# Optimization experiments

Hardware: AMD Instinct MI355X
Metric: run time of the kernel (lower is better)

Reference implementation:

```python
import jax, jax.numpy as jnp
import numpy as np

B, T, I, H, O = 128, 512, 512, 2048, 512  # batch, seq_length, input, hidden, output


def setup_inputs() -> dict:
    key = jax.random.key(0)
    ks = jax.random.split(key, 8)
    s_ih = 1.0 / np.sqrt(H)  # torch RNNCell/Linear default init scale 1/sqrt(hidden)
    body = jax.random.normal(ks[0], (B, T - 1, I), dtype=jnp.float32)
    # last timestep row stores the integer pad index (as float), per the module's protocol
    pad = jax.random.randint(ks[1], (B,), 0, T - 2)
    last = jnp.broadcast_to(pad[:, None, None].astype(jnp.float32), (B, 1, I))
    x = jnp.concatenate([body, last], axis=1)  # [B, T, I]
    W_ih = jax.random.uniform(ks[2], (H, I), jnp.float32, -s_ih, s_ih)
    W_hh = jax.random.uniform(ks[3], (H, H), jnp.float32, -s_ih, s_ih)
    b_ih = jax.random.uniform(ks[4], (H,), jnp.float32, -s_ih, s_ih)
    b_hh = jax.random.uniform(ks[5], (H,), jnp.float32, -s_ih, s_ih)
    W_fc = jax.random.uniform(ks[6], (O, H), jnp.float32, -s_ih, s_ih)
    b_fc = jax.random.uniform(ks[7], (O,), jnp.float32, -s_ih, s_ih)
    h0 = jnp.ones((H,), jnp.float32)  # self.h parameter, ones-initialized
    return {"x": x, "h0": h0, "W_ih": W_ih, "b_ih": b_ih, "W_hh": W_hh,
            "b_hh": b_hh, "W_fc": W_fc, "b_fc": b_fc}


def reference(x, h0, W_ih, b_ih, W_hh, b_hh, W_fc, b_fc):
    steps = T - 2  # loop runs over x.shape[2]-1 = (T-1)-1 timesteps
    pad = x[:, -1, 0].astype(jnp.int32)          # [B] pad indices
    xs = jnp.transpose(x[:, :steps, :], (1, 0, 2))  # [steps, B, I]
    h_init = jnp.broadcast_to(h0, (x.shape[0], H))  # self.h * ones([B,1])

    def step(h, xt):
        h = jnp.tanh(xt @ W_ih.T + b_ih + h @ W_hh.T + b_hh)
        return h, h @ W_fc.T + b_fc

    _, outs = jax.lax.scan(step, h_init, xs)     # [steps, B, O]
    # mask selects the single timestep j == pad_len[b]; everything else is zeroed
    mask = (pad[None, :] == jnp.arange(steps)[:, None]).astype(outs.dtype)  # [steps, B]
    return jnp.sum(outs * mask[:, :, None], axis=0)  # [B, O]
```

## Files before the change

kernel.cpp:

```cpp
#include <hip/hip_runtime.h>

#define Bsz 128
#define Tsz 512
#define Isz 512
#define Hsz 2048
#define Osz 512
#define STEPS 510

typedef short short8 __attribute__((ext_vector_type(8)));
typedef float floatx4 __attribute__((ext_vector_type(4)));

__device__ __forceinline__ unsigned short f2bf(float f) {
  unsigned int u = __builtin_bit_cast(unsigned int, f);
  u += 0x7FFFu + ((u >> 16) & 1u);
  return (unsigned short)(u >> 16);
}

__device__ __forceinline__ float tanh_fast(float x) {
  const float e = __expf(2.f * x);
  return 1.f - 2.f * __builtin_amdgcn_rcpf(e + 1.f);
}

template <int AUX>
__device__ __forceinline__ void gload_lds16(const void* g, void* l) {
  __builtin_amdgcn_global_load_lds(
      (const __attribute__((address_space(1))) void*)g,
      (__attribute__((address_space(3))) void*)l, 16, 0, AUX);
}

#define HCHUNK(c, enc)                                                                         \
  {                                                                                            \
    __builtin_amdgcn_s_waitcnt(enc);                                                           \
    const int hb = wvoff + (c) * 1024 + m16 * 64;                                              \
    const short8 a0 = *reinterpret_cast<const short8*>(&h_lds[hb + (quad ^ m7) * 8]);          \
    acc[0] = __builtin_amdgcn_mfma_f32_16x16x32_bf16(a0, wf[(c) * 2][0], acc[0], 0, 0, 0);     \
    acc[1] = __builtin_amdgcn_mfma_f32_16x16x32_bf16(a0, wf[(c) * 2][1], acc[1], 0, 0, 0);     \
    acc[2] = __builtin_amdgcn_mfma_f32_16x16x32_bf16(a0, wf[(c) * 2][2], acc[2], 0, 0, 0);     \
    acc[3] = __builtin_amdgcn_mfma_f32_16x16x32_bf16(a0, wf[(c) * 2][3], acc[3], 0, 0, 0);     \
    const short8 a1 = *reinterpret_cast<const short8*>(&h_lds[hb + ((4 + quad) ^ m7) * 8]);    \
    acc[0] = __builtin_amdgcn_mfma_f32_16x16x32_bf16(a1, wf[(c) * 2 + 1][0], acc[0], 0, 0, 0); \
    acc[1] = __builtin_amdgcn_mfma_f32_16x16x32_bf16(a1, wf[(c) * 2 + 1][1], acc[1], 0, 0, 0); \
    acc[2] = __builtin_amdgcn_mfma_f32_16x16x32_bf16(a1, wf[(c) * 2 + 1][2], acc[2], 0, 0, 0); \
    acc[3] = __builtin_amdgcn_mfma_f32_16x16x32_bf16(a1, wf[(c) * 2 + 1][3], acc[3], 0, 0, 0); \
  }

__global__ __launch_bounds__(256, 1)
void rnn_kernel(const float* __restrict__ x, const float* __restrict__ h0v,
                const float* __restrict__ W_ih, const float* __restrict__ b_ih,
                const float* __restrict__ W_hh, const float* __restrict__ b_hh,
                unsigned short* __restrict__ hbuf,
                float* __restrict__ hfinal,
                unsigned int* __restrict__ flags,
                unsigned int* __restrict__ xcc_arr)
{
  __shared__ short h_lds[4 * 8192];
  __shared__ float red_lds[4 * 1024];
  __shared__ int pad_lds[16];
  __shared__ unsigned int mode_lds;

  const int tid = threadIdx.x;
  const int lane = tid & 63;
  const int wv = tid >> 6;
  const int m16 = lane & 15;
  const int quad = lane >> 4;
  const int m7 = m16 & 7;
  const int rg = blockIdx.x & 7;
  const int cg = blockIdx.x >> 3;
  const int b0 = rg * 16;
  const int c0 = cg * 64;
  const int kq = wv * 512;
  const int kqx = wv * 128;
  const int wvoff = wv * 8192;

  {
    unsigned int xcc;
    asm volatile("s_getreg_b32 %0, hwreg(HW_REG_XCC_ID)" : "=s"(xcc));
    if (tid == 0)
      __hip_atomic_store(&xcc_arr[rg * 32 + cg], xcc + 1u, __ATOMIC_RELAXED,
                         __HIP_MEMORY_SCOPE_AGENT);
    if (wv == 0) {
      const unsigned int* ap = &xcc_arr[rg * 32 + (lane & 31)];
      unsigned int v;
      do {
        v = __hip_atomic_load(ap, __ATOMIC_RELAXED, __HIP_MEMORY_SCOPE_AGENT);
        if (__all((int)(v != 0u))) break;
        __builtin_amdgcn_s_sleep(2);
      } while (true);
      const int same = __all((int)(v == xcc + 1u));
      if (tid == 0) mode_lds = (unsigned int)same;
    }
  }

  short8 wf[16][4];
  short8 wih[4][4];
#pragma unroll
  for (int nt = 0; nt < 4; ++nt) {
    const int wrow = c0 + nt * 16 + m16;
    const float* base = W_hh + (size_t)wrow * Hsz + kq + quad * 8;
#pragma unroll
    for (int kc = 0; kc < 16; ++kc) {
      short8 v;
#pragma unroll
      for (int j = 0; j < 8; ++j) v[j] = (short)f2bf(base[kc * 32 + j]);
      wf[kc][nt] = v;
    }
    const float* basex = W_ih + (size_t)wrow * Isz + kqx + quad * 8;
#pragma unroll
    for (int kc = 0; kc < 4; ++kc) {
      short8 v;
#pragma unroll
      for (int j = 0; j < 8; ++j) v[j] = (short)f2bf(basex[kc * 32 + j]);
      wih[kc][nt] = v;
    }
  }

  const int rrow = tid >> 4;
  const int rcb = (tid & 15) * 4;
  float bias[4];
#pragma unroll
  for (int i = 0; i < 4; ++i) bias[i] = b_ih[c0 + rcb + i] + b_hh[c0 + rcb + i];

  if (tid < 16)
    pad_lds[tid] = (int)x[(size_t)(b0 + tid) * (Tsz * Isz) + (size_t)(Tsz - 1) * Isz];

  for (int i = lane; i < 1024; i += 64) {
    const int c = i >> 7;
    const int r = (i >> 3) & 15;
    const int u = i & 7;
    const int k = kq + c * 64 + u * 8;
    short8 v;
#pragma unroll
    for (int j = 0; j < 8; ++j) v[j] = (short)f2bf(h0v[k + j]);
    *reinterpret_cast<short8*>(&h_lds[wvoff + c * 1024 + r * 64 + (u ^ (r & 7)) * 8]) = v;
  }

  __syncthreads();
  const bool use_l2 = (mode_lds != 0u);

  const unsigned int* fp = flags + (size_t)(wv * 8 + (lane & 7)) * 8 + rg;

  for (int t = 0; t < STEPS; ++t) {
    const bool have_next = (t + 1) < STEPS;

    const float* xp = x + (size_t)(b0 + m16) * (Tsz * Isz) + (size_t)t * Isz + kqx + quad * 8;
    float4 xv[8];
#pragma unroll
    for (int kcc = 0; kcc < 4; ++kcc) {
      xv[2 * kcc] = *reinterpret_cast<const float4*>(xp + kcc * 32);
      xv[2 * kcc + 1] = *reinterpret_cast<const float4*>(xp + kcc * 32 + 4);
    }

    if (t > 0) {
      while (!__all((int)(__hip_atomic_load(fp, __ATOMIC_RELAXED,
                                            __HIP_MEMORY_SCOPE_AGENT) >= (unsigned)t)))
        __builtin_amdgcn_s_sleep(1);
      const unsigned short* hsrcp = hbuf + (size_t)(t & 1) * (Bsz * Hsz);
      if (use_l2) {
#pragma unroll
        for (int c = 0; c < 8; ++c) {
          const unsigned short* src = hsrcp + (size_t)((wv * 8 + c) * 8 + rg) * 1024;
          gload_lds16<0x01>(src + lane * 8, &h_lds[wvoff + c * 1024]);
          gload_lds16<0x01>(src + 512 + lane * 8, &h_lds[wvoff + c * 1024 + 512]);
        }
      } else {
#pragma unroll
        for (int c = 0; c < 8; ++c) {
          const unsigned short* src = hsrcp + (size_t)((wv * 8 + c) * 8 + rg) * 1024;
          gload_lds16<0x11>(src + lane * 8, &h_lds[wvoff + c * 1024]);
          gload_lds16<0x11>(src + 512 + lane * 8, &h_lds[wvoff + c * 1024 + 512]);
        }
      }
    }

    short8 xa[4];
#pragma unroll
    for (int kcc = 0; kcc < 4; ++kcc) {
      short8 a;
      a[0] = (short)f2bf(xv[2 * kcc].x);
      a[1] = (short)f2bf(xv[2 * kcc].y);
      a[2] = (short)f2bf(xv[2 * kcc].z);
      a[3] = (short)f2bf(xv[2 * kcc].w);
      a[4] = (short)f2bf(xv[2 * kcc + 1].x);
      a[5] = (short)f2bf(xv[2 * kcc + 1].y);
      a[6] = (short)f2bf(xv[2 * kcc + 1].z);
      a[7] = (short)f2bf(xv[2 * kcc + 1].w);
      xa[kcc] = a;
    }

    floatx4 acc[4];
#pragma unroll
    for (int nt = 0; nt < 4; ++nt) {
      floatx4 zero = {0.f, 0.f, 0.f, 0.f};
      acc[nt] = zero;
    }
#pragma unroll
    for (int kcc = 0; kcc < 4; ++kcc)
#pragma unroll
      for (int nt = 0; nt < 4; ++nt)
        acc[nt] = __builtin_amdgcn_mfma_f32_16x16x32_bf16(xa[kcc], wih[kcc][nt], acc[nt], 0, 0, 0);

    HCHUNK(0, 0x0F7E)
    HCHUNK(1, 0x0F7C)
    HCHUNK(2, 0x0F7A)
    HCHUNK(3, 0x0F78)
    HCHUNK(4, 0x0F76)
    HCHUNK(5, 0x0F74)
    HCHUNK(6, 0x0F72)
    HCHUNK(7, 0x0F70)

#pragma unroll
    for (int nt = 0; nt < 4; ++nt)
#pragma unroll
      for (int i = 0; i < 4; ++i)
        red_lds[wv * 1024 + (quad * 4 + i) * 64 + nt * 16 + m16] = acc[nt][i];

    __syncthreads();

    {
      float4 z = {0.f, 0.f, 0.f, 0.f};
#pragma unroll
      for (int ww = 0; ww < 4; ++ww) {
        const float4 p =
            *reinterpret_cast<const float4*>(&red_lds[ww * 1024 + rrow * 64 + rcb]);
        z.x += p.x; z.y += p.y; z.z += p.z; z.w += p.w;
      }
      const float t0 = tanh_fast(z.x + bias[0]);
      const float t1 = tanh_fast(z.y + bias[1]);
      const float t2 = tanh_fast(z.z + bias[2]);
      const float t3 = tanh_fast(z.w + bias[3]);
      unsigned long long pk = (unsigned long long)f2bf(t0) |
                              ((unsigned long long)f2bf(t1) << 16) |
                              ((unsigned long long)f2bf(t2) << 32) |
                              ((unsigned long long)f2bf(t3) << 48);
      const int toff = rrow * 64 + ((rcb >> 3) ^ (rrow & 7)) * 8 + ((rcb >> 2) & 1) * 4;
      unsigned short* hd = hbuf + (size_t)((t + 1) & 1) * (Bsz * Hsz) +
                           (size_t)(cg * 8 + rg) * 1024 + toff;
      if (use_l2) {
        *reinterpret_cast<unsigned long long*>(hd) = pk;
      } else {
        __hip_atomic_store(reinterpret_cast<unsigned long long*>(hd), pk,
                           __ATOMIC_RELAXED, __HIP_MEMORY_SCOPE_AGENT);
      }
      if (pad_lds[rrow] == t) {
        float4 o;
        o.x = t0; o.y = t1; o.z = t2; o.w = t3;
        *reinterpret_cast<float4*>(&hfinal[(size_t)(b0 + rrow) * Hsz + c0 + rcb]) = o;
      }
    }

    __syncthreads();

    if (have_next && tid == 0) {
      __hip_atomic_store(flags + cg * 8 + rg, (unsigned)(t + 1),
                         __ATOMIC_RELAXED, __HIP_MEMORY_SCOPE_AGENT);
    }
  }
}

__global__ __launch_bounds__(64)
void fc_kernel(const float* __restrict__ hfinal, const float* __restrict__ W_fc,
               const float* __restrict__ b_fc, float* __restrict__ out) {
  const int lane = threadIdx.x & 63;
  const int m16 = lane & 15;
  const int quad = lane >> 4;
  const int b0 = (blockIdx.x & 7) * 16;
  const int o0 = (blockIdx.x >> 3) * 16;
  floatx4 acc = {0.f, 0.f, 0.f, 0.f};
  const float* ap = hfinal + (size_t)(b0 + m16) * Hsz + quad * 8;
  const float* bp = W_fc + (size_t)(o0 + m16) * Hsz + quad * 8;
#pragma unroll 4
  for (int kc = 0; kc < 64; ++kc) {
    short8 a, b;
#pragma unroll
    for (int j = 0; j < 8; ++j) a[j] = (short)f2bf(ap[kc * 32 + j]);
#pragma unroll
    for (int j = 0; j < 8; ++j) b[j] = (short)f2bf(bp[kc * 32 + j]);
    acc = __builtin_amdgcn_mfma_f32_16x16x32_bf16(a, b, acc, 0, 0, 0);
  }
  const float bias = b_fc[o0 + m16];
#pragma unroll
  for (int i = 0; i < 4; ++i)
    out[(size_t)(b0 + quad * 4 + i) * Osz + o0 + m16] = acc[i] + bias;
}

__global__ void zero_flags(unsigned int* f) { f[blockIdx.x * 256 + threadIdx.x] = 0u; }

extern "C" void kernel_launch(void* const* d_in, const int* in_sizes, int n_in,
                              void* d_out, int out_size, void* d_ws, size_t ws_size,
                              hipStream_t stream) {
  const float* x = (const float*)d_in[0];
  const float* h0 = (const float*)d_in[1];
  const float* W_ih = (const float*)d_in[2];
  const float* b_ih = (const float*)d_in[3];
  const float* W_hh = (const float*)d_in[4];
  const float* b_hh = (const float*)d_in[5];
  const float* W_fc = (const float*)d_in[6];
  const float* b_fc = (const float*)d_in[7];
  float* out = (float*)d_out;

  char* ws = (char*)d_ws;
  unsigned short* hbuf = (unsigned short*)ws;
  float* hfinal = (float*)(ws + (1u << 20));
  unsigned int* flags = (unsigned int*)(ws + (2u << 20));
  unsigned int* xcc_arr = flags + 256;

  zero_flags<<<2, 256, 0, stream>>>(flags);
  rnn_kernel<<<256, 256, 0, stream>>>(x, h0, W_ih, b_ih, W_hh, b_hh, hbuf, hfinal,
                                      flags, xcc_arr);
  fc_kernel<<<256, 64, 0, stream>>>(hfinal, W_fc, b_fc, out);
}
```

Before: 2.069 ms.

## Split RNN block K-reduction across eight waves instead of four

Doubles the threads per block to 512 so each wave handles half the hidden and input reduction slice. Register-resident W_hh/W_ih fragments per wave shrink, and the per-step MFMA chain and h loads per wave halve. The cost is an eight-way LDS cross-wave reduction with narrower float2 epilogue stores, plus more flag polling per wave. Because 512 threads share one CU, the register budget per wave also tightens.

```diff
diff --git a/kernel.cpp b/kernel.cpp
--- a/kernel.cpp
+++ b/kernel.cpp
@@ -44,7 +44,7 @@
     acc[3] = __builtin_amdgcn_mfma_f32_16x16x32_bf16(a1, wf[(c) * 2 + 1][3], acc[3], 0, 0, 0); \
   }
 
-__global__ __launch_bounds__(256, 1)
+__global__ __launch_bounds__(512, 2)
 void rnn_kernel(const float* __restrict__ x, const float* __restrict__ h0v,
                 const float* __restrict__ W_ih, const float* __restrict__ b_ih,
                 const float* __restrict__ W_hh, const float* __restrict__ b_hh,
@@ -53,8 +53,8 @@
                 unsigned int* __restrict__ flags,
                 unsigned int* __restrict__ xcc_arr)
 {
-  __shared__ short h_lds[4 * 8192];
-  __shared__ float red_lds[4 * 1024];
+  __shared__ short h_lds[8 * 4096];
+  __shared__ float red_lds[8 * 1024];
   __shared__ int pad_lds[16];
   __shared__ unsigned int mode_lds;
 
@@ -68,9 +68,9 @@
   const int cg = blockIdx.x >> 3;
   const int b0 = rg * 16;
   const int c0 = cg * 64;
-  const int kq = wv * 512;
-  const int kqx = wv * 128;
-  const int wvoff = wv * 8192;
+  const int kq = wv * 256;
+  const int kqx = wv * 64;
+  const int wvoff = wv * 4096;
 
   {
     unsigned int xcc;
@@ -91,14 +91,14 @@
     }
   }
 
-  short8 wf[16][4];
-  short8 wih[4][4];
+  short8 wf[8][4];
+  short8 wih[2][4];
 #pragma unroll
   for (int nt = 0; nt < 4; ++nt) {
     const int wrow = c0 + nt * 16 + m16;
     const float* base = W_hh + (size_t)wrow * Hsz + kq + quad * 8;
 #pragma unroll
-    for (int kc = 0; kc < 16; ++kc) {
+    for (int kc = 0; kc < 8; ++kc) {
       short8 v;
 #pragma unroll
       for (int j = 0; j < 8; ++j) v[j] = (short)f2bf(base[kc * 32 + j]);
@@ -106,7 +106,7 @@
     }
     const float* basex = W_ih + (size_t)wrow * Isz + kqx + quad * 8;
 #pragma unroll
-    for (int kc = 0; kc < 4; ++kc) {
+    for (int kc = 0; kc < 2; ++kc) {
       short8 v;
 #pragma unroll
       for (int j = 0; j < 8; ++j) v[j] = (short)f2bf(basex[kc * 32 + j]);
@@ -114,16 +114,15 @@
     }
   }
 
-  const int rrow = tid >> 4;
-  const int rcb = (tid & 15) * 4;
-  float bias[4];
-#pragma unroll
-  for (int i = 0; i < 4; ++i) bias[i] = b_ih[c0 + rcb + i] + b_hh[c0 + rcb + i];
+  const int rrow = tid >> 5;
+  const int cb = (tid & 31) * 2;
+  const float bias0 = b_ih[c0 + cb] + b_hh[c0 + cb];
+  const float bias1 = b_ih[c0 + cb + 1] + b_hh[c0 + cb + 1];
 
   if (tid < 16)
     pad_lds[tid] = (int)x[(size_t)(b0 + tid) * (Tsz * Isz) + (size_t)(Tsz - 1) * Isz];
 
-  for (int i = lane; i < 1024; i += 64) {
+  for (int i = lane; i < 512; i += 64) {
     const int c = i >> 7;
     const int r = (i >> 3) & 15;
     const int u = i & 7;
@@ -137,15 +136,15 @@
   __syncthreads();
   const bool use_l2 = (mode_lds != 0u);
 
-  const unsigned int* fp = flags + (size_t)(wv * 8 + (lane & 7)) * 8 + rg;
+  const unsigned int* fp = flags + (size_t)(wv * 4 + (lane & 3)) * 8 + rg;
 
   for (int t = 0; t < STEPS; ++t) {
     const bool have_next = (t + 1) < STEPS;
 
     const float* xp = x + (size_t)(b0 + m16) * (Tsz * Isz) + (size_t)t * Isz + kqx + quad * 8;
-    float4 xv[8];
-#pragma unroll
-    for (int kcc = 0; kcc < 4; ++kcc) {
+    float4 xv[4];
+#pragma unroll
+    for (int kcc = 0; kcc < 2; ++kcc) {
       xv[2 * kcc] = *reinterpret_cast<const float4*>(xp + kcc * 32);
       xv[2 * kcc + 1] = *reinterpret_cast<const float4*>(xp + kcc * 32 + 4);
     }
@@ -157,24 +156,24 @@
       const unsigned short* hsrcp = hbuf + (size_t)(t & 1) * (Bsz * Hsz);
       if (use_l2) {
 #pragma unroll
-        for (int c = 0; c < 8; ++c) {
-          const unsigned short* src = hsrcp + (size_t)((wv * 8 + c) * 8 + rg) * 1024;
+        for (int c = 0; c < 4; ++c) {
+          const unsigned short* src = hsrcp + (size_t)((wv * 4 + c) * 8 + rg) * 1024;
           gload_lds16<0x01>(src + lane * 8, &h_lds[wvoff + c * 1024]);
           gload_lds16<0x01>(src + 512 + lane * 8, &h_lds[wvoff + c * 1024 + 512]);
         }
       } else {
 #pragma unroll
-        for (int c = 0; c < 8; ++c) {
-          const unsigned short* src = hsrcp + (size_t)((wv * 8 + c) * 8 + rg) * 1024;
+        for (int c = 0; c < 4; ++c) {
+          const unsigned short* src = hsrcp + (size_t)((wv * 4 + c) * 8 + rg) * 1024;
           gload_lds16<0x11>(src + lane * 8, &h_lds[wvoff + c * 1024]);
           gload_lds16<0x11>(src + 512 + lane * 8, &h_lds[wvoff + c * 1024 + 512]);
         }
       }
     }
 
-    short8 xa[4];
-#pragma unroll
-    for (int kcc = 0; kcc < 4; ++kcc) {
+    short8 xa[2];
+#pragma unroll
+    for (int kcc = 0; kcc < 2; ++kcc) {
       short8 a;
       a[0] = (short)f2bf(xv[2 * kcc].x);
       a[1] = (short)f2bf(xv[2 * kcc].y);
@@ -194,19 +193,15 @@
       acc[nt] = zero;
     }
 #pragma unroll
-    for (int kcc = 0; kcc < 4; ++kcc)
+    for (int kcc = 0; kcc < 2; ++kcc)
 #pragma unroll
       for (int nt = 0; nt < 4; ++nt)
         acc[nt] = __builtin_amdgcn_mfma_f32_16x16x32_bf16(xa[kcc], wih[kcc][nt], acc[nt], 0, 0, 0);
 
-    HCHUNK(0, 0x0F7E)
-    HCHUNK(1, 0x0F7C)
-    HCHUNK(2, 0x0F7A)
-    HCHUNK(3, 0x0F78)
-    HCHUNK(4, 0x0F76)
-    HCHUNK(5, 0x0F74)
-    HCHUNK(6, 0x0F72)
-    HCHUNK(7, 0x0F70)
+    HCHUNK(0, 0x0F76)
+    HCHUNK(1, 0x0F74)
+    HCHUNK(2, 0x0F72)
+    HCHUNK(3, 0x0F70)
 
 #pragma unroll
     for (int nt = 0; nt < 4; ++nt)
@@ -217,34 +212,30 @@
     __syncthreads();
 
     {
-      float4 z = {0.f, 0.f, 0.f, 0.f};
-#pragma unroll
-      for (int ww = 0; ww < 4; ++ww) {
-        const float4 p =
-            *reinterpret_cast<const float4*>(&red_lds[ww * 1024 + rrow * 64 + rcb]);
-        z.x += p.x; z.y += p.y; z.z += p.z; z.w += p.w;
+      float z0 = 0.f, z1 = 0.f;
+#pragma unroll
+      for (int ww = 0; ww < 8; ++ww) {
+        const float2 p =
+            *reinterpret_cast<const float2*>(&red_lds[ww * 1024 + rrow * 64 + cb]);
+        z0 += p.x; z1 += p.y;
       }
-      const float t0 = tanh_fast(z.x + bias[0]);
-      const float t1 = tanh_fast(z.y + bias[1]);
-      const float t2 = tanh_fast(z.z + bias[2]);
-      const float t3 = tanh_fast(z.w + bias[3]);
-      unsigned long long pk = (unsigned long long)f2bf(t0) |
-                              ((unsigned long long)f2bf(t1) << 16) |
-                              ((unsigned long long)f2bf(t2) << 32) |
-                              ((unsigned long long)f2bf(t3) << 48);
-      const int toff = rrow * 64 + ((rcb >> 3) ^ (rrow & 7)) * 8 + ((rcb >> 2) & 1) * 4;
+      const float t0 = tanh_fast(z0 + bias0);
+      const float t1 = tanh_fast(z1 + bias1);
+      const unsigned int pk =
+          (unsigned int)f2bf(t0) | ((unsigned int)f2bf(t1) << 16);
+      const int toff = rrow * 64 + ((cb >> 3) ^ (rrow & 7)) * 8 + (cb & 7);
       unsigned short* hd = hbuf + (size_t)((t + 1) & 1) * (Bsz * Hsz) +
                            (size_t)(cg * 8 + rg) * 1024 + toff;
       if (use_l2) {
-        *reinterpret_cast<unsigned long long*>(hd) = pk;
+        *reinterpret_cast<unsigned int*>(hd) = pk;
       } else {
-        __hip_atomic_store(reinterpret_cast<unsigned long long*>(hd), pk,
+        __hip_atomic_store(reinterpret_cast<unsigned int*>(hd), pk,
                            __ATOMIC_RELAXED, __HIP_MEMORY_SCOPE_AGENT);
       }
       if (pad_lds[rrow] == t) {
-        float4 o;
-        o.x = t0; o.y = t1; o.z = t2; o.w = t3;
-        *reinterpret_cast<float4*>(&hfinal[(size_t)(b0 + rrow) * Hsz + c0 + rcb]) = o;
+        float2 o;
+        o.x = t0; o.y = t1;
+        *reinterpret_cast<float2*>(&hfinal[(size_t)(b0 + rrow) * Hsz + c0 + cb]) = o;
       }
     }
 
@@ -305,7 +296,7 @@
   unsigned int* xcc_arr = flags + 256;
 
   zero_flags<<<2, 256, 0, stream>>>(flags);
-  rnn_kernel<<<256, 256, 0, stream>>>(x, h0, W_ih, b_ih, W_hh, b_hh, hbuf, hfinal,
+  rnn_kernel<<<256, 512, 0, stream>>>(x, h0, W_ih, b_ih, W_hh, b_hh, hbuf, hfinal,
                                       flags, xcc_arr);
   fc_kernel<<<256, 64, 0, stream>>>(hfinal, W_fc, b_fc, out);
 }
```

After: 2.768 ms. 33.8% more time.

## Assign row/column tiles to blocks dynamically by XCD to co-locate row groups

Applied to the files above, without the earlier changes.

Instead of mapping blockIdx directly to (row group, column group), each block reads its hardware XCC ID and claims a tile slot on that XCD through atomic counters, so all 32 blocks of a row group try to land on the same XCD. Blocks that overflow an XCD's 32 slots wait for all blocks to register, then claim leftover tiles with compare-exchange. The aim is to make the per-step cross-block hidden-state exchange stay within one XCD's L2, which makes the existing same-XCC fast path usable more often. It adds a startup atomic phase, a global spin barrier and extra workspace that must be zeroed.

```diff
diff --git a/kernel.cpp b/kernel.cpp
--- a/kernel.cpp
+++ b/kernel.cpp
@@ -51,12 +51,16 @@
                 unsigned short* __restrict__ hbuf,
                 float* __restrict__ hfinal,
                 unsigned int* __restrict__ flags,
-                unsigned int* __restrict__ xcc_arr)
+                unsigned int* __restrict__ xcc_arr,
+                unsigned int* __restrict__ claimed,
+                unsigned int* __restrict__ xcd_cnt,
+                unsigned int* __restrict__ done_cnt)
 {
   __shared__ short h_lds[4 * 8192];
   __shared__ float red_lds[4 * 1024];
   __shared__ int pad_lds[16];
   __shared__ unsigned int mode_lds;
+  __shared__ int rgcg_lds;
 
   const int tid = threadIdx.x;
   const int lane = tid & 63;
@@ -64,8 +68,47 @@
   const int m16 = lane & 15;
   const int quad = lane >> 4;
   const int m7 = m16 & 7;
-  const int rg = blockIdx.x & 7;
-  const int cg = blockIdx.x >> 3;
+
+  unsigned int xcc;
+  asm volatile("s_getreg_b32 %0, hwreg(HW_REG_XCC_ID)" : "=s"(xcc));
+  xcc &= 7u;
+  if (tid == 0) {
+    const unsigned int slot = __hip_atomic_fetch_add(&xcd_cnt[xcc], 1u,
+                                                     __ATOMIC_RELAXED,
+                                                     __HIP_MEMORY_SCOPE_AGENT);
+    int myrg, mycg;
+    if (slot < 32u) {
+      myrg = (int)xcc; mycg = (int)slot;
+      __hip_atomic_store(&claimed[myrg * 32 + mycg], 1u, __ATOMIC_RELAXED,
+                         __HIP_MEMORY_SCOPE_AGENT);
+      asm volatile("s_waitcnt vmcnt(0)" ::: "memory");
+      __hip_atomic_fetch_add(done_cnt, 1u, __ATOMIC_RELAXED,
+                             __HIP_MEMORY_SCOPE_AGENT);
+    } else {
+      __hip_atomic_fetch_add(done_cnt, 1u, __ATOMIC_RELAXED,
+                             __HIP_MEMORY_SCOPE_AGENT);
+      while (__hip_atomic_load(done_cnt, __ATOMIC_RELAXED,
+                               __HIP_MEMORY_SCOPE_AGENT) < 256u)
+        __builtin_amdgcn_s_sleep(2);
+      myrg = -1; mycg = 0;
+      for (int j = 0;; j = (j + 1) & 255) {
+        if (__hip_atomic_load(&claimed[j], __ATOMIC_RELAXED,
+                              __HIP_MEMORY_SCOPE_AGENT) == 0u) {
+          unsigned int exp = 0u;
+          if (__hip_atomic_compare_exchange_strong(
+                  &claimed[j], &exp, 1u, __ATOMIC_RELAXED, __ATOMIC_RELAXED,
+                  __HIP_MEMORY_SCOPE_AGENT)) {
+            myrg = j >> 5; mycg = j & 31;
+            break;
+          }
+        }
+      }
+    }
+    rgcg_lds = (myrg << 8) | mycg;
+  }
+  __syncthreads();
+  const int rg = rgcg_lds >> 8;
+  const int cg = rgcg_lds & 255;
   const int b0 = rg * 16;
   const int c0 = cg * 64;
   const int kq = wv * 512;
@@ -73,8 +116,6 @@
   const int wvoff = wv * 8192;
 
   {
-    unsigned int xcc;
-    asm volatile("s_getreg_b32 %0, hwreg(HW_REG_XCC_ID)" : "=s"(xcc));
     if (tid == 0)
       __hip_atomic_store(&xcc_arr[rg * 32 + cg], xcc + 1u, __ATOMIC_RELAXED,
                          __HIP_MEMORY_SCOPE_AGENT);
@@ -303,9 +344,12 @@
   float* hfinal = (float*)(ws + (1u << 20));
   unsigned int* flags = (unsigned int*)(ws + (2u << 20));
   unsigned int* xcc_arr = flags + 256;
-
-  zero_flags<<<2, 256, 0, stream>>>(flags);
+  unsigned int* claimed = flags + 512;
+  unsigned int* xcd_cnt = flags + 768;
+  unsigned int* done_cnt = flags + 776;
+
+  zero_flags<<<4, 256, 0, stream>>>(flags);
   rnn_kernel<<<256, 256, 0, stream>>>(x, h0, W_ih, b_ih, W_hh, b_hh, hbuf, hfinal,
-                                      flags, xcc_arr);
+                                      flags, xcc_arr, claimed, xcd_cnt, done_cnt);
   fc_kernel<<<256, 64, 0, stream>>>(hfinal, W_fc, b_fc, out);
 }
```

Measured after the change: 2.101 ms. About the same (+1.6%).
